# Performance work log

Measured on AMD Instinct MI355X. Metric: run time of the kernel, lower is better.

Reference implementation:

```python
import jax, jax.numpy as jnp
import numpy as np

N, M_CHE, M_VDW, B = 20000, 20, 20, 200
H, E, NODE_IN, NCONV = 128, 20, 13, 3
CHE_CUTOFF, VDW_CUTOFF = 8.0, 12.0


def setup_inputs() -> dict:
    key = jax.random.key(0)
    ks = jax.random.split(key, 16)
    s = 0.05
    inp = {}
    inp['atoms_embed'] = jax.random.normal(ks[0], (N, NODE_IN), jnp.float32)
    inp['che_nbrs_fea'] = jax.random.uniform(ks[1], (N, M_CHE), jnp.float32, 0.5, CHE_CUTOFF * 1.1)
    inp['vdw_nbrs_fea'] = jax.random.uniform(ks[2], (N, M_VDW), jnp.float32, 0.5, VDW_CUTOFF * 1.1)
    inp['che_nbrs_idx'] = jax.random.randint(ks[3], (N, M_CHE), 0, N)
    inp['vdw_nbrs_idx'] = jax.random.randint(ks[4], (N, M_VDW), 0, N)
    inp['num_atoms'] = jnp.full((B,), N // B, dtype=jnp.int32)  # 200 crystals x 100 atoms
    inp['emb_W'] = jax.random.normal(ks[5], (NODE_IN, H), jnp.float32) * s
    inp['emb_b'] = jnp.zeros((H,), jnp.float32)
    inp['che_filter_W'] = jax.random.normal(ks[6], (NCONV, E, H), jnp.float32) * s
    inp['che_filter_b'] = jnp.zeros((NCONV, H), jnp.float32)
    inp['che_fc_W'] = jax.random.normal(ks[7], (NCONV, 3 * H, 2 * H), jnp.float32) * s
    inp['che_fc_b'] = jnp.zeros((NCONV, 2 * H), jnp.float32)
    inp['vdw_filter_W'] = jax.random.normal(ks[8], (NCONV, E, H), jnp.float32) * s
    inp['vdw_filter_b'] = jnp.zeros((NCONV, H), jnp.float32)
    inp['vdw_fc_W'] = jax.random.normal(ks[9], (NCONV, 3 * H, 2 * H), jnp.float32) * s
    inp['vdw_fc_b'] = jnp.zeros((NCONV, 2 * H), jnp.float32)
    inp['fc1_W'] = jax.random.normal(ks[10], (H, H), jnp.float32) * s
    inp['fc1_b'] = jnp.zeros((H,), jnp.float32)
    inp['out_W'] = jax.random.normal(ks[11], (H, 1), jnp.float32) * s
    inp['out_b'] = jnp.zeros((1,), jnp.float32)
    return inp


def _rbf(d, cutoff):
    # sinc-like radial basis with cosine envelope; zero beyond cutoff
    k = jnp.arange(1, E + 1, dtype=d.dtype)  # [E]
    de = d[..., None]  # [N, M, 1]
    r = jnp.where(de < cutoff, jnp.sin(de * k * (jnp.pi / cutoff)) / de, jnp.zeros((), d.dtype))
    env = 0.5 * (jnp.cos(jnp.pi * d / cutoff) + 1.0)
    return r * env[..., None]  # [N, M, E]


def _conv_half(nodes, rbf_e, idx, fW, fb, gW, gb):
    n, m = idx.shape
    edges = rbf_e @ fW + fb  # [N, M, H]
    self_fea = jnp.broadcast_to(nodes[:, None, :], (n, m, nodes.shape[1]))
    total = jnp.concatenate([self_fea, edges, nodes[idx]], axis=2)  # [N, M, 3H]
    gated = total @ gW + gb  # [N, M, 2H]
    filt, core = jnp.split(gated, 2, axis=2)
    return jnp.sum(jax.nn.sigmoid(filt) * jax.nn.softplus(core), axis=1)  # [N, H]


def reference(atoms_embed, che_nbrs_fea, che_nbrs_idx, vdw_nbrs_fea, vdw_nbrs_idx,
              num_atoms, emb_W, emb_b, che_filter_W, che_filter_b, che_fc_W, che_fc_b,
              vdw_filter_W, vdw_filter_b, vdw_fc_W, vdw_fc_b, fc1_W, fc1_b, out_W, out_b):
    nodes = atoms_embed @ emb_W + emb_b  # [N, H]
    che_rbf = _rbf(che_nbrs_fea, CHE_CUTOFF)
    vdw_rbf = _rbf(vdw_nbrs_fea, VDW_CUTOFF)
    for i in range(NCONV):
        che = _conv_half(nodes, che_rbf, che_nbrs_idx, che_filter_W[i], che_filter_b[i], che_fc_W[i], che_fc_b[i])
        vdw = _conv_half(nodes, vdw_rbf, vdw_nbrs_idx, vdw_filter_W[i], vdw_filter_b[i], vdw_fc_W[i], vdw_fc_b[i])
        nodes = jax.nn.softplus(nodes + che + vdw)
    # per-crystal mean pooling from contiguous atom ranges given by num_atoms
    ends = jnp.cumsum(num_atoms)
    seg = jnp.searchsorted(ends, jnp.arange(nodes.shape[0]), side='right')
    sums = jax.ops.segment_sum(nodes, seg, num_segments=B)
    crys = sums / num_atoms[:, None].astype(nodes.dtype)  # [B, H]
    crys = jax.nn.softplus(jax.nn.softplus(crys) @ fc1_W + fc1_b)
    predict = (crys @ out_W + out_b)[:, 0]  # [B]
    return predict
```

## Files before the change

### kernel.cpp

```cpp
#include <hip/hip_runtime.h>
#include <hip/hip_bf16.h>
#include <math.h>

#define NN 20000
#define MM 20
#define EE 20
#define HH 128
#define BB 200
#define NCONV 3
#define CHE_CUT 8.0f
#define VDW_CUT 12.0f
#define PI_F 3.14159265358979323846f
#define LOG2E_F 1.44269504088896340736f
#define LN2_F 0.69314718055994530942f

typedef __fp16 half2_t __attribute__((ext_vector_type(2)));
typedef _Float16 f16x8 __attribute__((ext_vector_type(8)));
typedef float f32x4 __attribute__((ext_vector_type(4)));

__device__ __forceinline__ float exp2_(float x) {
#if __has_builtin(__builtin_amdgcn_exp2f)
    return __builtin_amdgcn_exp2f(x);
#else
    return exp2f(x);
#endif
}
__device__ __forceinline__ float log2_(float x) {
#if __has_builtin(__builtin_amdgcn_logf)
    return __builtin_amdgcn_logf(x);
#else
    return log2f(x);
#endif
}
__device__ __forceinline__ float rcp_(float x) {
#if __has_builtin(__builtin_amdgcn_rcpf)
    return __builtin_amdgcn_rcpf(x);
#else
    return 1.f / x;
#endif
}
__device__ __forceinline__ float sp_(float x) {
    return (x > 15.f) ? x : LN2_F * log2_(1.f + exp2_(x * LOG2E_F));
}
__device__ __forceinline__ float fdot2_(half2_t a, half2_t b, float c) {
#if __has_builtin(__builtin_amdgcn_fdot2)
    return __builtin_amdgcn_fdot2(a, b, c, false);
#else
    return (float)a.x * (float)b.x + (float)a.y * (float)b.y + c;
#endif
}

__global__ void prep_bias(const float* __restrict__ cfb, const float* __restrict__ cgW,
                          const float* __restrict__ cgb,
                          const float* __restrict__ vfb, const float* __restrict__ vgW,
                          const float* __restrict__ vgb, float* __restrict__ bc) {
    int half = blockIdx.y;
    int l = blockIdx.z;
    int j = threadIdx.x;
    const float* fb = half ? vfb : cfb;
    const float* gW = half ? vgW : cgW;
    const float* gb = half ? vgb : cgb;
    const float* gWe = gW + ((size_t)l * 384 + 128) * 256;
    const float* brow = fb + (size_t)l * HH;
    float acc = gb[(size_t)l * 256 + j];
    for (int k = 0; k < HH; ++k) acc = fmaf(brow[k], gWe[k * 256 + j], acc);
    bc[((size_t)l * 2 + half) * 256 + j] = acc * LOG2E_F;
}

__global__ void prep_bwc(const float* __restrict__ cfW, const float* __restrict__ cgW,
                         const float* __restrict__ vfW, const float* __restrict__ vgW,
                         _Float16* __restrict__ bwc) {
    int nt = blockIdx.x;
    int half = blockIdx.y;
    int l = blockIdx.z;
    int tid = threadIdx.x;
    int k = tid >> 4, nc = tid & 15;
    int t = (nt & 7) * 16 + nc;
    int gcol = (nt >> 3) * 128 + t;
    const float* fW = half ? vfW : cfW;
    const float* gW = half ? vgW : cgW;
    const float* gWe = gW + ((size_t)l * 384 + 128) * 256;
    float val = 0.f;
    if (k < EE) {
        const float* frow = fW + ((size_t)l * EE + k) * HH;
        for (int kk = 0; kk < HH; ++kk) val = fmaf(frow[kk], gWe[kk * 256 + gcol], val);
        val *= LOG2E_F;
    }
    bwc[(((size_t)(l * 2 + half) * 16 + nt) * 64 + (k >> 3) * 16 + nc) * 8 + (k & 7)] = (_Float16)val;
}

__global__ void prep_bpk(const float* __restrict__ cgW, const float* __restrict__ vgW,
                         _Float16* __restrict__ bpk) {
    int i = blockIdx.x * 256 + threadIdx.x;
    if (i >= NCONV * 128 * 1024) return;
    int l = i >> 17;
    int rem = i & 131071;
    int k = rem >> 10;
    int c = rem & 1023;
    int half = (c >> 8) & 1;
    const float* src = half ? vgW : cgW;
    int grow = l * 384 + ((c < 512) ? k : 256 + k);
    float val = src[(size_t)grow * 256 + (c & 255)] * LOG2E_F;
    int nt = c >> 4, nc = c & 15;
    int s = k >> 5, kq = (k >> 3) & 3, j = k & 7;
    bpk[(size_t)l * 131072 + (((size_t)nt * 4 + s) * 64 + kq * 16 + nc) * 8 + j] = (_Float16)val;
}

__global__ void embed_kernel(const float* __restrict__ atoms, const float* __restrict__ W,
                             const float* __restrict__ bias, float* __restrict__ nodes,
                             _Float16* __restrict__ nodes_h) {
    int n = blockIdx.x, t = threadIdx.x;
    const float* arow = atoms + (size_t)n * 13;
    float acc = bias[t];
    #pragma unroll
    for (int k = 0; k < 13; ++k) acc = fmaf(arow[k], W[k * HH + t], acc);
    nodes[(size_t)n * HH + t] = acc;
    nodes_h[(size_t)n * HH + t] = (_Float16)acc;
}

__global__ void rbf_kernel(const float* __restrict__ che_fea, const float* __restrict__ vdw_fea,
                           _Float16* __restrict__ rfrag) {
    int i = blockIdx.x * blockDim.x + threadIdx.x;
    if (i >= 2 * NN * MM) {
        int j = i - 2 * NN * MM;
        if (j >= 2 * NN * 12) return;
        int la = 4 + (j % 12);
        int hn = j / 12;
        _Float16* base = rfrag + (((size_t)hn * 2 + 1) * 64) * 8 + la * 8;
        f16x8 z = {};
        *(f16x8*)(base) = z;
        *(f16x8*)(base + 128) = z;
        *(f16x8*)(base + 256) = z;
        *(f16x8*)(base + 384) = z;
        return;
    }
    bool isv = i >= NN * MM;
    int rem = isv ? i - NN * MM : i;
    int n = rem / MM, m = rem % MM;
    float d = isv ? vdw_fea[rem] : che_fea[rem];
    float cutoff = isv ? VDW_CUT : CHE_CUT;
    float x = d * (PI_F / cutoff);
    float s1 = sinf(x), c1 = cosf(x);
    float env = 0.5f * (c1 + 1.f);
    float scale = (d < cutoff) ? (env / d) : 0.f;
    float out[EE];
    float skm1 = 0.f, sk = s1;
    #pragma unroll
    for (int e = 0; e < EE; ++e) {
        out[e] = sk * scale;
        float nx = 2.f * c1 * sk - skm1;
        skm1 = sk; sk = nx;
    }
    int mt = m >> 4, la = m & 15;
    _Float16* base = rfrag + (((size_t)(isv ? NN + n : n) * 2 + mt) * 64) * 8 + la * 8;
    f16x8 v0, v1, v2, v3;
    #pragma unroll
    for (int j = 0; j < 8; ++j) {
        v0[j] = (_Float16)out[j];
        v1[j] = (_Float16)out[8 + j];
        v2[j] = (j < 4) ? (_Float16)out[16 + j] : (_Float16)0.f;
        v3[j] = (_Float16)0.f;
    }
    *(f16x8*)(base) = v0;
    *(f16x8*)(base + 128) = v1;
    *(f16x8*)(base + 256) = v2;
    *(f16x8*)(base + 384) = v3;
}

__global__ __launch_bounds__(256)
void gemm_mfma(const _Float16* __restrict__ Ah, const _Float16* __restrict__ Bpk,
               half2_t* __restrict__ Spk, half2_t* __restrict__ Ypk) {
    int lane = threadIdx.x & 63;
    int wv = threadIdx.x >> 6;
    int m0 = blockIdx.x * 16;
    int la = lane & 15;
    int quad = lane >> 4;
    int k0 = quad * 8;

    f16x8 af[4];
    {
        const _Float16* arow = Ah + (size_t)(m0 + la) * 128 + k0;
        #pragma unroll
        for (int s = 0; s < 4; ++s)
            af[s] = *(const f16x8*)(arow + s * 32);
    }

    const f16x8* bp = (const f16x8*)Bpk;
    int ntf0 = wv * 16;
    half2_t* dst = (wv & 2) ? Ypk : Spk;
    int wbase = (wv & 1) * 128 + la;

    f16x8 fb[4], cb[4], nfb[4], ncb[4];
    #pragma unroll
    for (int s = 0; s < 4; ++s) {
        fb[s] = bp[((size_t)ntf0 * 4 + s) * 64 + lane];
        cb[s] = bp[((size_t)(ntf0 + 8) * 4 + s) * 64 + lane];
    }
    for (int p = 0; p < 8; ++p) {
        if (p < 7) {
            #pragma unroll
            for (int s = 0; s < 4; ++s) {
                nfb[s] = bp[((size_t)(ntf0 + p + 1) * 4 + s) * 64 + lane];
                ncb[s] = bp[((size_t)(ntf0 + 9 + p) * 4 + s) * 64 + lane];
            }
        }
        f32x4 accf = {0.f, 0.f, 0.f, 0.f};
        f32x4 accc = {0.f, 0.f, 0.f, 0.f};
        #pragma unroll
        for (int s = 0; s < 4; ++s) {
            accf = __builtin_amdgcn_mfma_f32_16x16x32_f16(af[s], fb[s], accf, 0, 0, 0);
            accc = __builtin_amdgcn_mfma_f32_16x16x32_f16(af[s], cb[s], accc, 0, 0, 0);
        }
        int row = m0 + quad * 4;
        int word = wbase + p * 16;
        #pragma unroll
        for (int i = 0; i < 4; ++i) {
            half2_t pk = __builtin_amdgcn_cvt_pkrtz(accf[i], accc[i]);
            dst[(size_t)(row + i) * 256 + word] = pk;
        }
        #pragma unroll
        for (int s = 0; s < 4; ++s) { fb[s] = nfb[s]; cb[s] = ncb[s]; }
    }
}

#define GSTRIDE 132
__global__ __launch_bounds__(256)
void edge_kernel(const float* __restrict__ nodes_in, float* __restrict__ nodes_out,
                 _Float16* __restrict__ nodes_h,
                 const half2_t* __restrict__ Spk, const half2_t* __restrict__ Ypk,
                 const _Float16* __restrict__ rfrag,
                 const int* __restrict__ idx_che, const int* __restrict__ idx_vdw,
                 const _Float16* __restrict__ bwc,
                 const float* __restrict__ bC) {
    __shared__ half2_t G2[40 * GSTRIDE];
    __shared__ float red[HH];
    int t = threadIdx.x;
    int lane = t & 63;
    int wv = t >> 6;
    int n = blockIdx.x;
    int h2 = t >> 7;
    int tc = t & 127;

    const int* idxp = h2 ? (idx_vdw + (size_t)n * MM) : (idx_che + (size_t)n * MM);
    int jx[MM];
    #pragma unroll
    for (int m = 0; m < MM; ++m) jx[m] = idxp[m];

    half2_t yw[MM];
    #pragma unroll
    for (int m = 0; m < MM; ++m) yw[m] = Ypk[(size_t)jx[m] * 256 + h2 * 128 + tc];

    half2_t spx = Spk[(size_t)n * 256 + h2 * 128 + tc];
    float old = (h2 == 0) ? nodes_in[(size_t)n * HH + tc] : 0.f;
    float sf = bC[h2 * 256 + tc] + (float)spx.x;
    float sc = bC[h2 * 256 + 128 + tc] + (float)spx.y;

    const half2_t ONE0 = {(__fp16)1.f, (__fp16)0.f};
    const half2_t ZERO1 = {(__fp16)0.f, (__fp16)1.f};
    int quad = lane >> 4;
    int cla = lane & 15;

    {
        int hw = wv >> 1;
        int rbase = hw * 20;
        const _Float16* rf = rfrag + ((size_t)(hw * NN + n) * 2) * 512;
        f16x8 a0 = *(const f16x8*)(rf + lane * 8);
        f16x8 a1 = *(const f16x8*)(rf + 512 + lane * 8);
        const f16x8* bw = (const f16x8*)bwc + ((size_t)hw * 16) * 64;
        #pragma unroll
        for (int p = 0; p < 4; ++p) {
            int pg = (wv & 1) * 4 + p;
            f16x8 bf = bw[(size_t)pg * 64 + lane];
            f16x8 bcfr = bw[(size_t)(8 + pg) * 64 + lane];
            f32x4 g0f = {0.f, 0.f, 0.f, 0.f};
            f32x4 g0c = {0.f, 0.f, 0.f, 0.f};
            f32x4 g1f = {0.f, 0.f, 0.f, 0.f};
            f32x4 g1c = {0.f, 0.f, 0.f, 0.f};
            g0f = __builtin_amdgcn_mfma_f32_16x16x32_f16(a0, bf, g0f, 0, 0, 0);
            g0c = __builtin_amdgcn_mfma_f32_16x16x32_f16(a0, bcfr, g0c, 0, 0, 0);
            g1f = __builtin_amdgcn_mfma_f32_16x16x32_f16(a1, bf, g1f, 0, 0, 0);
            g1c = __builtin_amdgcn_mfma_f32_16x16x32_f16(a1, bcfr, g1c, 0, 0, 0);
            int base = pg * 16 + cla;
            #pragma unroll
            for (int i = 0; i < 4; ++i)
                G2[(rbase + quad * 4 + i) * GSTRIDE + base] = __builtin_amdgcn_cvt_pkrtz(g0f[i], g0c[i]);
            if (quad == 0) {
                #pragma unroll
                for (int i = 0; i < 4; ++i)
                    G2[(rbase + 16 + i) * GSTRIDE + base] = __builtin_amdgcn_cvt_pkrtz(g1f[i], g1c[i]);
            }
        }
    }
    __syncthreads();

    float acc = 0.f;
    const half2_t* gp = &G2[(h2 * 20) * GSTRIDE + tc];
    #pragma unroll
    for (int m = 0; m < MM; ++m) {
        half2_t gw = gp[m * GSTRIDE] + yw[m];
        float gf = fdot2_(gw, ONE0, sf);
        float gc = fdot2_(gw, ZERO1, sc);
        float uu = rcp_(1.f + exp2_(-gf));
        float p = log2_(1.f + exp2_(gc));
        p = (gc > 24.f) ? gc : p;
        acc = fmaf(p, uu, acc);
    }
    if (h2) red[tc] = acc;
    __syncthreads();
    if (!h2) {
        float res = sp_(fmaf(acc + red[tc], LN2_F, old));
        nodes_out[(size_t)n * HH + tc] = res;
        nodes_h[(size_t)n * HH + tc] = (_Float16)res;
    }
}

__global__ void pool_kernel(const float* __restrict__ nodes, const int* __restrict__ num_atoms,
                            const float* __restrict__ fc1_W, const float* __restrict__ fc1_b,
                            const float* __restrict__ out_W, const float* __restrict__ out_b,
                            float* __restrict__ out) {
    __shared__ float sh[HH];
    __shared__ float red[HH];
    int b = blockIdx.x, t = threadIdx.x;
    int start = 0;
    for (int i = 0; i < b; ++i) start += num_atoms[i];
    int cnt = num_atoms[b];
    float sum = 0.f;
    for (int a = 0; a < cnt; ++a) sum += nodes[(size_t)(start + a) * HH + t];
    float mean = sum / (float)cnt;
    sh[t] = sp_(mean);
    __syncthreads();
    float o = fc1_b[t];
    #pragma unroll 4
    for (int k = 0; k < HH; ++k) o = fmaf(sh[k], fc1_W[k * HH + t], o);
    red[t] = sp_(o) * out_W[t];
    __syncthreads();
    if (t == 0) {
        float tot = 0.f;
        for (int k = 0; k < HH; ++k) tot += red[k];
        out[b] = tot + out_b[0];
    }
}

extern "C" void kernel_launch(void* const* d_in, const int* in_sizes, int n_in,
                              void* d_out, int out_size, void* d_ws, size_t ws_size,
                              hipStream_t stream) {
    const float* atoms_embed   = (const float*)d_in[0];
    const float* che_nbrs_fea  = (const float*)d_in[1];
    const float* vdw_nbrs_fea  = (const float*)d_in[2];
    const int*   che_nbrs_idx  = (const int*)  d_in[3];
    const int*   vdw_nbrs_idx  = (const int*)  d_in[4];
    const int*   num_atoms     = (const int*)  d_in[5];
    const float* emb_W         = (const float*)d_in[6];
    const float* emb_b         = (const float*)d_in[7];
    const float* che_filter_W  = (const float*)d_in[8];
    const float* che_filter_b  = (const float*)d_in[9];
    const float* che_fc_W      = (const float*)d_in[10];
    const float* che_fc_b      = (const float*)d_in[11];
    const float* vdw_filter_W  = (const float*)d_in[12];
    const float* vdw_filter_b  = (const float*)d_in[13];
    const float* vdw_fc_W      = (const float*)d_in[14];
    const float* vdw_fc_b      = (const float*)d_in[15];
    const float* fc1_W         = (const float*)d_in[16];
    const float* fc1_b         = (const float*)d_in[17];
    const float* out_W         = (const float*)d_in[18];
    const float* out_b         = (const float*)d_in[19];
    float* out = (float*)d_out;

    float* w = (float*)d_ws;
    float* nodesA   = w;
    float* nodesB   = nodesA + (size_t)NN * HH;
    _Float16* nodes_h = (_Float16*)(nodesB + (size_t)NN * HH);
    half2_t* Spk    = (half2_t*)(nodes_h + (size_t)NN * HH);
    half2_t* Ypk    = Spk + (size_t)NN * 256;
    _Float16* rfrag = (_Float16*)(Ypk + (size_t)NN * 256);
    _Float16* bpk   = rfrag + (size_t)2 * NN * 2 * 512;
    _Float16* bwc   = bpk + (size_t)NCONV * 131072;
    float* bc       = (float*)(bwc + (size_t)NCONV * 2 * 16 * 512);

    prep_bias<<<dim3(1, 2, NCONV), 256, 0, stream>>>(
        che_filter_b, che_fc_W, che_fc_b, vdw_filter_b, vdw_fc_W, vdw_fc_b, bc);
    prep_bwc<<<dim3(16, 2, NCONV), 512, 0, stream>>>(
        che_filter_W, che_fc_W, vdw_filter_W, vdw_fc_W, bwc);
    prep_bpk<<<(NCONV * 128 * 1024 + 255) / 256, 256, 0, stream>>>(che_fc_W, vdw_fc_W, bpk);
    embed_kernel<<<NN, HH, 0, stream>>>(atoms_embed, emb_W, emb_b, nodesA, nodes_h);
    rbf_kernel<<<(2 * NN * MM + 2 * NN * 12 + 255) / 256, 256, 0, stream>>>(
        che_nbrs_fea, vdw_nbrs_fea, rfrag);

    float* cur = nodesA;
    float* nxt = nodesB;
    for (int l = 0; l < NCONV; ++l) {
        gemm_mfma<<<NN / 16, 256, 0, stream>>>(nodes_h, bpk + (size_t)l * 131072, Spk, Ypk);
        edge_kernel<<<NN, 256, 0, stream>>>(
            cur, nxt, nodes_h, Spk, Ypk, rfrag, che_nbrs_idx, vdw_nbrs_idx,
            bwc + (size_t)l * 2 * 16 * 512, bc + (size_t)l * 512);
        float* tmp = cur; cur = nxt; nxt = tmp;
    }

    pool_kernel<<<BB, HH, 0, stream>>>(cur, num_atoms, fc1_W, fc1_b, out_W, out_b, out);
}
```

Baseline: 493.2 us.

## Double GEMM rows per block, scalarize neighbor indices, repack edge LDS layout

The node GEMM now computes 32 rows per block instead of 16, so each B fragment loaded from global memory feeds twice as many MFMAs and half as many blocks are launched. The edge kernel loads neighbor indices through readfirstlane so they live in scalar registers and the gather addresses become scalar-based. The LDS tile is relaid out so each thread reads two adjacent neighbors per row, the gating loop is unrolled in pairs, and the softplus overflow branch becomes a min/max clamp. These changes trade more registers in the GEMM and a different LDS bank pattern for fewer loads and less vector address arithmetic.

Result: slower. 518.2 us (+5.1%).

```diff
diff --git a/kernel.cpp b/kernel.cpp
--- a/kernel.cpp
+++ b/kernel.cpp
@@ -48,6 +48,11 @@
 #else
     return (float)a.x * (float)b.x + (float)a.y * (float)b.y + c;
 #endif
+}
+__device__ __forceinline__ unsigned long long uniform_u64(unsigned long long v) {
+    unsigned int lo = (unsigned int)__builtin_amdgcn_readfirstlane((int)(unsigned int)v);
+    unsigned int hi = (unsigned int)__builtin_amdgcn_readfirstlane((int)(unsigned int)(v >> 32));
+    return ((unsigned long long)hi << 32) | lo;
 }
 
 __global__ void prep_bias(const float* __restrict__ cfb, const float* __restrict__ cgW,
@@ -172,17 +177,19 @@
                half2_t* __restrict__ Spk, half2_t* __restrict__ Ypk) {
     int lane = threadIdx.x & 63;
     int wv = threadIdx.x >> 6;
-    int m0 = blockIdx.x * 16;
+    int m0 = blockIdx.x * 32;
     int la = lane & 15;
     int quad = lane >> 4;
     int k0 = quad * 8;
 
-    f16x8 af[4];
+    f16x8 af0[4], af1[4];
     {
         const _Float16* arow = Ah + (size_t)(m0 + la) * 128 + k0;
         #pragma unroll
-        for (int s = 0; s < 4; ++s)
-            af[s] = *(const f16x8*)(arow + s * 32);
+        for (int s = 0; s < 4; ++s) {
+            af0[s] = *(const f16x8*)(arow + s * 32);
+            af1[s] = *(const f16x8*)(arow + 2048 + s * 32);
+        }
     }
 
     const f16x8* bp = (const f16x8*)Bpk;
@@ -204,26 +211,30 @@
                 ncb[s] = bp[((size_t)(ntf0 + 9 + p) * 4 + s) * 64 + lane];
             }
         }
-        f32x4 accf = {0.f, 0.f, 0.f, 0.f};
-        f32x4 accc = {0.f, 0.f, 0.f, 0.f};
+        f32x4 a0f = {0.f, 0.f, 0.f, 0.f};
+        f32x4 a0c = {0.f, 0.f, 0.f, 0.f};
+        f32x4 a1f = {0.f, 0.f, 0.f, 0.f};
+        f32x4 a1c = {0.f, 0.f, 0.f, 0.f};
         #pragma unroll
         for (int s = 0; s < 4; ++s) {
-            accf = __builtin_amdgcn_mfma_f32_16x16x32_f16(af[s], fb[s], accf, 0, 0, 0);
-            accc = __builtin_amdgcn_mfma_f32_16x16x32_f16(af[s], cb[s], accc, 0, 0, 0);
+            a0f = __builtin_amdgcn_mfma_f32_16x16x32_f16(af0[s], fb[s], a0f, 0, 0, 0);
+            a0c = __builtin_amdgcn_mfma_f32_16x16x32_f16(af0[s], cb[s], a0c, 0, 0, 0);
+            a1f = __builtin_amdgcn_mfma_f32_16x16x32_f16(af1[s], fb[s], a1f, 0, 0, 0);
+            a1c = __builtin_amdgcn_mfma_f32_16x16x32_f16(af1[s], cb[s], a1c, 0, 0, 0);
         }
         int row = m0 + quad * 4;
         int word = wbase + p * 16;
         #pragma unroll
         for (int i = 0; i < 4; ++i) {
-            half2_t pk = __builtin_amdgcn_cvt_pkrtz(accf[i], accc[i]);
-            dst[(size_t)(row + i) * 256 + word] = pk;
+            dst[(size_t)(row + i) * 256 + word] = __builtin_amdgcn_cvt_pkrtz(a0f[i], a0c[i]);
+            dst[(size_t)(row + 16 + i) * 256 + word] = __builtin_amdgcn_cvt_pkrtz(a1f[i], a1c[i]);
         }
         #pragma unroll
         for (int s = 0; s < 4; ++s) { fb[s] = nfb[s]; cb[s] = ncb[s]; }
     }
 }
 
-#define GSTRIDE 132
+#define G2P 258
 __global__ __launch_bounds__(256)
 void edge_kernel(const float* __restrict__ nodes_in, float* __restrict__ nodes_out,
                  _Float16* __restrict__ nodes_h,
@@ -232,7 +243,7 @@
                  const int* __restrict__ idx_che, const int* __restrict__ idx_vdw,
                  const _Float16* __restrict__ bwc,
                  const float* __restrict__ bC) {
-    __shared__ half2_t G2[40 * GSTRIDE];
+    __shared__ half2_t G2[20 * G2P];
     __shared__ float red[HH];
     int t = threadIdx.x;
     int lane = t & 63;
@@ -242,13 +253,15 @@
     int tc = t & 127;
 
     const int* idxp = h2 ? (idx_vdw + (size_t)n * MM) : (idx_che + (size_t)n * MM);
+    const int* idxs = (const int*)uniform_u64((unsigned long long)idxp);
     int jx[MM];
     #pragma unroll
-    for (int m = 0; m < MM; ++m) jx[m] = idxp[m];
-
+    for (int m = 0; m < MM; ++m) jx[m] = __builtin_amdgcn_readfirstlane(idxs[m]);
+
+    const half2_t* yb = (const half2_t*)uniform_u64((unsigned long long)(Ypk + h2 * 128));
     half2_t yw[MM];
     #pragma unroll
-    for (int m = 0; m < MM; ++m) yw[m] = Ypk[(size_t)jx[m] * 256 + h2 * 128 + tc];
+    for (int m = 0; m < MM; ++m) yw[m] = yb[(size_t)jx[m] * 256 + tc];
 
     half2_t spx = Spk[(size_t)n * 256 + h2 * 128 + tc];
     float old = (h2 == 0) ? nodes_in[(size_t)n * HH + tc] : 0.f;
@@ -262,7 +275,6 @@
 
     {
         int hw = wv >> 1;
-        int rbase = hw * 20;
         const _Float16* rf = rfrag + ((size_t)(hw * NN + n) * 2) * 512;
         f16x8 a0 = *(const f16x8*)(rf + lane * 8);
         f16x8 a1 = *(const f16x8*)(rf + 512 + lane * 8);
@@ -280,30 +292,47 @@
             g0c = __builtin_amdgcn_mfma_f32_16x16x32_f16(a0, bcfr, g0c, 0, 0, 0);
             g1f = __builtin_amdgcn_mfma_f32_16x16x32_f16(a1, bf, g1f, 0, 0, 0);
             g1c = __builtin_amdgcn_mfma_f32_16x16x32_f16(a1, bcfr, g1c, 0, 0, 0);
-            int base = pg * 16 + cla;
-            #pragma unroll
-            for (int i = 0; i < 4; ++i)
-                G2[(rbase + quad * 4 + i) * GSTRIDE + base] = __builtin_amdgcn_cvt_pkrtz(g0f[i], g0c[i]);
+            int col = pg * 16 + cla;
+            half2_t* w0 = &G2[(hw * 10 + quad * 2) * G2P + col * 2];
+            w0[0] = __builtin_amdgcn_cvt_pkrtz(g0f[0], g0c[0]);
+            w0[1] = __builtin_amdgcn_cvt_pkrtz(g0f[1], g0c[1]);
+            half2_t* w1 = &G2[(hw * 10 + quad * 2 + 1) * G2P + col * 2];
+            w1[0] = __builtin_amdgcn_cvt_pkrtz(g0f[2], g0c[2]);
+            w1[1] = __builtin_amdgcn_cvt_pkrtz(g0f[3], g0c[3]);
             if (quad == 0) {
-                #pragma unroll
-                for (int i = 0; i < 4; ++i)
-                    G2[(rbase + 16 + i) * GSTRIDE + base] = __builtin_amdgcn_cvt_pkrtz(g1f[i], g1c[i]);
+                half2_t* w2 = &G2[(hw * 10 + 8) * G2P + col * 2];
+                w2[0] = __builtin_amdgcn_cvt_pkrtz(g1f[0], g1c[0]);
+                w2[1] = __builtin_amdgcn_cvt_pkrtz(g1f[1], g1c[1]);
+                half2_t* w3 = &G2[(hw * 10 + 9) * G2P + col * 2];
+                w3[0] = __builtin_amdgcn_cvt_pkrtz(g1f[2], g1c[2]);
+                w3[1] = __builtin_amdgcn_cvt_pkrtz(g1f[3], g1c[3]);
             }
         }
     }
     __syncthreads();
 
     float acc = 0.f;
-    const half2_t* gp = &G2[(h2 * 20) * GSTRIDE + tc];
-    #pragma unroll
-    for (int m = 0; m < MM; ++m) {
-        half2_t gw = gp[m * GSTRIDE] + yw[m];
-        float gf = fdot2_(gw, ONE0, sf);
-        float gc = fdot2_(gw, ZERO1, sc);
-        float uu = rcp_(1.f + exp2_(-gf));
-        float p = log2_(1.f + exp2_(gc));
-        p = (gc > 24.f) ? gc : p;
-        acc = fmaf(p, uu, acc);
+    const half2_t* gq = G2 + (h2 * 10) * G2P + tc * 2;
+    #pragma unroll
+    for (int mb = 0; mb < 10; ++mb) {
+        half2_t ga = gq[mb * G2P];
+        half2_t gb = gq[mb * G2P + 1];
+        half2_t gw0 = ga + yw[2 * mb];
+        half2_t gw1 = gb + yw[2 * mb + 1];
+        float gf0 = fdot2_(gw0, ONE0, sf);
+        float gc0 = fdot2_(gw0, ZERO1, sc);
+        float gf1 = fdot2_(gw1, ONE0, sf);
+        float gc1 = fdot2_(gw1, ZERO1, sc);
+        float ef0 = exp2_(-gf0), ec0 = exp2_(gc0);
+        float ef1 = exp2_(-gf1), ec1 = exp2_(gc1);
+        float u0 = rcp_(1.f + ef0);
+        float u1 = rcp_(1.f + ef1);
+        float p0 = log2_(1.f + ec0);
+        float p1 = log2_(1.f + ec1);
+        p0 = fminf(p0, fmaxf(gc0, 25.f));
+        p1 = fminf(p1, fmaxf(gc1, 25.f));
+        acc = fmaf(p0, u0, acc);
+        acc = fmaf(p1, u1, acc);
     }
     if (h2) red[tc] = acc;
     __syncthreads();
@@ -389,7 +418,7 @@
     float* cur = nodesA;
     float* nxt = nodesB;
     for (int l = 0; l < NCONV; ++l) {
-        gemm_mfma<<<NN / 16, 256, 0, stream>>>(nodes_h, bpk + (size_t)l * 131072, Spk, Ypk);
+        gemm_mfma<<<NN / 32, 256, 0, stream>>>(nodes_h, bpk + (size_t)l * 131072, Spk, Ypk);
         edge_kernel<<<NN, 256, 0, stream>>>(
             cur, nxt, nodes_h, Spk, Ypk, rfrag, che_nbrs_idx, vdw_nbrs_idx,
             bwc + (size_t)l * 2 * 16 * 512, bc + (size_t)l * 512);
```
